# Kernel optimization log

Hardware: AMD Instinct MI355X
Metric: run time of the kernel (lower is better)

The kernel has to match this reference:

```python
import jax, jax.numpy as jnp
import numpy as np

N_NODES = 100000
N_EDGES = 400000
N_GRAPHS = 4096
IN_DIM = 128
HID = 64
HEADS = 8
NEG_SLOPE = 0.2


def setup_inputs() -> dict:
    key = jax.random.key(0)
    ks = jax.random.split(key, 12)
    x = jax.random.normal(ks[0], (N_NODES, IN_DIM), dtype=jnp.float32)
    edge_index = jax.random.randint(ks[1], (2, N_EDGES), 0, N_NODES, dtype=jnp.int64)
    batch = jnp.sort(jax.random.randint(ks[2], (N_NODES,), 0, N_GRAPHS, dtype=jnp.int64))
    s = 1.0 / np.sqrt(IN_DIM)
    W1 = jax.random.normal(ks[3], (IN_DIM, HEADS * HID), dtype=jnp.float32) * s
    att_src1 = jax.random.normal(ks[4], (HEADS, HID), dtype=jnp.float32) * 0.1
    att_dst1 = jax.random.normal(ks[5], (HEADS, HID), dtype=jnp.float32) * 0.1
    b1 = jnp.zeros((HEADS * HID,), dtype=jnp.float32)
    s2 = 1.0 / np.sqrt(HEADS * HID)
    W2 = jax.random.normal(ks[6], (HEADS * HID, HID), dtype=jnp.float32) * s2
    att_src2 = jax.random.normal(ks[7], (1, HID), dtype=jnp.float32) * 0.1
    att_dst2 = jax.random.normal(ks[8], (1, HID), dtype=jnp.float32) * 0.1
    b2 = jnp.zeros((HID,), dtype=jnp.float32)
    Wf = jax.random.normal(ks[9], (HID, 1), dtype=jnp.float32) * (1.0 / np.sqrt(HID))
    bf = jnp.zeros((1,), dtype=jnp.float32)
    return {"x": x, "edge_index": edge_index, "batch": batch,
            "W1": W1, "att_src1": att_src1, "att_dst1": att_dst1, "b1": b1,
            "W2": W2, "att_src2": att_src2, "att_dst2": att_dst2, "b2": b2,
            "Wf": Wf, "bf": bf}


def _gat_layer(x, src, dst, W, att_src, att_dst, bias, heads, out_ch, concat):
    # PyG GATConv math (add_self_loops handled by caller via src/dst)
    n = x.shape[0]
    h = (x @ W).reshape(n, heads, out_ch)          # [N, H, C]
    a_s = (h * att_src[None]).sum(-1)               # [N, H]
    a_d = (h * att_dst[None]).sum(-1)               # [N, H]
    alpha = a_s[src] + a_d[dst]                     # [E, H]
    alpha = jax.nn.leaky_relu(alpha, NEG_SLOPE)
    amax = jax.ops.segment_max(alpha, dst, num_segments=n)
    alpha = jnp.exp(alpha - amax[dst])
    denom = jax.ops.segment_sum(alpha, dst, num_segments=n)
    alpha = alpha / (denom[dst] + 1e-16)
    msg = h[src] * alpha[:, :, None]                # [E, H, C]
    out = jax.ops.segment_sum(msg, dst, num_segments=n)  # [N, H, C]
    out = out.reshape(n, heads * out_ch) if concat else out.mean(axis=1)
    return out + bias


def reference(x, edge_index, batch, W1, att_src1, att_dst1, b1,
              W2, att_src2, att_dst2, b2, Wf, bf):
    n = x.shape[0]
    loop = jnp.arange(n, dtype=edge_index.dtype)
    src = jnp.concatenate([edge_index[0], loop])
    dst = jnp.concatenate([edge_index[1], loop])
    h = _gat_layer(x, src, dst, W1, att_src1, att_dst1, b1, HEADS, HID, True)
    h = jax.nn.relu(h)
    h = _gat_layer(h, src, dst, W2, att_src2, att_dst2, b2, 1, HID, False)
    h = jax.nn.relu(h)
    sums = jax.ops.segment_sum(h, batch, num_segments=N_GRAPHS)        # [G, HID]
    cnts = jax.ops.segment_sum(jnp.ones((n,), h.dtype), batch, num_segments=N_GRAPHS)
    pooled = sums / jnp.clip(cnts, 1.0)[:, None]
    return pooled @ Wf + bf
```

## Files before the change

kernel.cpp:

```cpp
#include <hip/hip_runtime.h>

typedef short bfrag8 __attribute__((ext_vector_type(8)));
typedef float f32x4 __attribute__((ext_vector_type(4)));
typedef unsigned int uint4v __attribute__((ext_vector_type(4)));

__device__ __forceinline__ unsigned short f2bf(float f) {
    unsigned u = __float_as_uint(f);
    u += 0x7fffu + ((u >> 16) & 1u);
    return (unsigned short)(u >> 16);
}
__device__ __forceinline__ float bf2f(unsigned short s) {
    return __uint_as_float((unsigned)s << 16);
}

__global__ __launch_bounds__(256) void zero_i32(int* __restrict__ p, int n) {
    int i = (int)(blockIdx.x * 256u + threadIdx.x);
    int stride = gridDim.x * 256;
    for (; i < n; i += stride) p[i] = 0;
}

__global__ __launch_bounds__(256) void cvt_f32_bf16(const float* __restrict__ in,
                                                    unsigned short* __restrict__ out, size_t n) {
    size_t i = (blockIdx.x * 256llu + threadIdx.x) * 4;
    size_t stride = (size_t)gridDim.x * 1024llu;
    for (; i < n; i += stride) {
        float4 v = *(const float4*)(in + i);
        out[i + 0] = f2bf(v.x);
        out[i + 1] = f2bf(v.y);
        out[i + 2] = f2bf(v.z);
        out[i + 3] = f2bf(v.w);
    }
}

__global__ __launch_bounds__(256) void prep_w1(const float* __restrict__ W1,
                                               unsigned short* __restrict__ out) {
    int i = (int)(blockIdx.x * 256u + threadIdx.x);
    if (i >= 8 * 4 * 4 * 64 * 8) return;
    int e = i & 7, l = (i >> 3) & 63, c = (i >> 9) & 3, s = (i >> 11) & 3, h = i >> 13;
    int k = s * 32 + (l >> 4) * 8 + e;
    int col = h * 64 + c * 16 + (l & 15);
    out[i] = f2bf(W1[k * 512 + col]);
}

__global__ __launch_bounds__(256) void prep_w2(const float* __restrict__ W2,
                                               unsigned short* __restrict__ out) {
    int i = (int)(blockIdx.x * 256u + threadIdx.x);
    if (i >= 16 * 4 * 64 * 8) return;
    int e = i & 7, l = (i >> 3) & 63, c = (i >> 9) & 3, s = i >> 11;
    int k = s * 32 + (l >> 4) * 8 + e;
    int col = c * 16 + (l & 15);
    out[i] = f2bf(W2[k * 64 + col]);
}

__global__ __launch_bounds__(256) void hist_kernel(const int* __restrict__ ei,
                                                   int* __restrict__ cnt, int E, int N) {
    int t = (int)(blockIdx.x * 256u + threadIdx.x);
    if (t >= E + N) return;
    int dst = (t < E) ? ei[E + t] : t - E;
    atomicAdd(cnt + dst, 1);
}

#define SCAN_BLK 2048
__global__ __launch_bounds__(256) void scan1(const int* __restrict__ cnt,
                                             int* __restrict__ rs,
                                             int* __restrict__ bsum, int N) {
    __shared__ int lds[256];
    int base = blockIdx.x * SCAN_BLK;
    int vals[8];
    int tsum = 0;
    int idx0 = base + threadIdx.x * 8;
#pragma unroll
    for (int j = 0; j < 8; ++j) {
        int i = idx0 + j;
        int v = (i < N) ? cnt[i] : 0;
        vals[j] = tsum;
        tsum += v;
    }
    lds[threadIdx.x] = tsum;
    __syncthreads();
    for (int off = 1; off < 256; off <<= 1) {
        int v = lds[threadIdx.x];
        int u = (threadIdx.x >= (unsigned)off) ? lds[threadIdx.x - off] : 0;
        __syncthreads();
        lds[threadIdx.x] = v + u;
        __syncthreads();
    }
    int texcl = (threadIdx.x == 0) ? 0 : lds[threadIdx.x - 1];
#pragma unroll
    for (int j = 0; j < 8; ++j) {
        int i = idx0 + j;
        if (i < N) rs[i] = texcl + vals[j];
    }
    if (threadIdx.x == 255) bsum[blockIdx.x] = lds[255];
}

__global__ void scan2(int* __restrict__ bsum, int* __restrict__ rs, int nb, int N) {
    if (threadIdx.x == 0 && blockIdx.x == 0) {
        int run = 0;
        for (int b = 0; b < nb; ++b) { int t = bsum[b]; bsum[b] = run; run += t; }
        rs[N] = run;
    }
}

__global__ __launch_bounds__(256) void scan3(int* __restrict__ rs,
                                             const int* __restrict__ bsum, int N) {
    int i = (int)(blockIdx.x * 256u + threadIdx.x);
    if (i < N) rs[i] += bsum[i / SCAN_BLK];
}

__global__ __launch_bounds__(256) void scatter_kernel(const int* __restrict__ ei,
                                                      const int* __restrict__ rs,
                                                      int* __restrict__ cur,
                                                      int* __restrict__ csrc, int E, int N) {
    int t = (int)(blockIdx.x * 256u + threadIdx.x);
    if (t >= E + N) return;
    int src, dst;
    if (t < E) { src = ei[t]; dst = ei[E + t]; } else { src = dst = t - E; }
    int pos = rs[dst] + atomicAdd(cur + dst, 1);
    csrc[pos] = src;
}

__global__ __launch_bounds__(256) void gstart_build(const int* __restrict__ batch,
                                                    int* __restrict__ gstart, int N, int G) {
    int i = (int)(blockIdx.x * 256u + threadIdx.x);
    if (i > N) return;
    if (i == N) {
        int p = batch[N - 1];
        for (int g = p + 1; g <= G; ++g) gstart[g] = N;
    } else {
        int b = batch[i];
        int p = (i == 0) ? -1 : batch[i - 1];
        for (int g = p + 1; g <= b; ++g) gstart[g] = i;
    }
}

__global__ __launch_bounds__(256) void gemm_l1(const unsigned short* __restrict__ A,
                                               const unsigned short* __restrict__ Bfrag,
                                               unsigned short* __restrict__ Cbf,
                                               int M, int ldc, int asStride,
                                               const float* __restrict__ avs,
                                               const float* __restrict__ avd,
                                               float* __restrict__ as_,
                                               float* __restrict__ ad_) {
    const int lane = threadIdx.x & 63;
    const int wave = threadIdx.x >> 6;
    const int l15 = lane & 15, l16 = lane >> 4;
    const int cb = blockIdx.y;
    const long rowBase = (long)blockIdx.x * 128 + wave * 32;

    bfrag8 bf[4][4];
    const bfrag8* bp = (const bfrag8*)(Bfrag + (size_t)cb * 8192);
#pragma unroll
    for (int s = 0; s < 4; ++s)
#pragma unroll
        for (int c = 0; c < 4; ++c)
            bf[s][c] = bp[(s * 4 + c) * 64 + lane];

    f32x4 acc[2][4];
#pragma unroll
    for (int r = 0; r < 2; ++r)
#pragma unroll
        for (int c = 0; c < 4; ++c)
#pragma unroll
            for (int e = 0; e < 4; ++e) acc[r][c][e] = 0.f;

    long r0 = rowBase + l15;        if (r0 > M - 1) r0 = M - 1;
    long r1 = rowBase + 16 + l15;   if (r1 > M - 1) r1 = M - 1;
    const unsigned short* a0p = A + r0 * 128 + l16 * 8;
    const unsigned short* a1p = A + r1 * 128 + l16 * 8;

#pragma unroll
    for (int s = 0; s < 4; ++s) {
        bfrag8 a0 = *(const bfrag8*)(a0p + s * 32);
        bfrag8 a1 = *(const bfrag8*)(a1p + s * 32);
#pragma unroll
        for (int c = 0; c < 4; ++c) {
            acc[0][c] = __builtin_amdgcn_mfma_f32_16x16x32_bf16(a0, bf[s][c], acc[0][c], 0, 0, 0);
            acc[1][c] = __builtin_amdgcn_mfma_f32_16x16x32_bf16(a1, bf[s][c], acc[1][c], 0, 0, 0);
        }
    }

    float avsv[4], avdv[4];
#pragma unroll
    for (int c = 0; c < 4; ++c) {
        avsv[c] = avs[cb * 64 + c * 16 + l15];
        avdv[c] = avd[cb * 64 + c * 16 + l15];
    }

#pragma unroll
    for (int r = 0; r < 2; ++r) {
#pragma unroll
        for (int reg = 0; reg < 4; ++reg) {
            long row = rowBase + r * 16 + l16 * 4 + reg;
            bool ok = row < M;
            float ps = 0.f, pd = 0.f;
#pragma unroll
            for (int c = 0; c < 4; ++c) {
                float v = acc[r][c][reg];
                if (ok) Cbf[row * ldc + cb * 64 + c * 16 + l15] = f2bf(v);
                ps += v * avsv[c];
                pd += v * avdv[c];
            }
#pragma unroll
            for (int off = 1; off < 16; off <<= 1) {
                ps += __shfl_xor(ps, off);
                pd += __shfl_xor(pd, off);
            }
            if (l15 == 0 && ok) {
                as_[row * asStride + cb] = ps;
                ad_[row * asStride + cb] = pd;
            }
        }
    }
}

__global__ __launch_bounds__(256) void gemm_l2_k512(const unsigned short* __restrict__ A,
                                                    const unsigned short* __restrict__ Bfrag,
                                                    unsigned short* __restrict__ Cbf,
                                                    int M,
                                                    const float* __restrict__ avs,
                                                    const float* __restrict__ avd,
                                                    float* __restrict__ as_,
                                                    float* __restrict__ ad_) {
    const int lane = threadIdx.x & 63;
    const int wave = threadIdx.x >> 6;
    const int l15 = lane & 15, l16 = lane >> 4;
    const long rowBase = (long)blockIdx.x * 128 + wave * 32;
    const bfrag8* bp = (const bfrag8*)Bfrag;

    f32x4 acc[2][4];
#pragma unroll
    for (int r = 0; r < 2; ++r)
#pragma unroll
        for (int c = 0; c < 4; ++c)
#pragma unroll
            for (int e = 0; e < 4; ++e) acc[r][c][e] = 0.f;

    long r0 = rowBase + l15;        if (r0 > M - 1) r0 = M - 1;
    long r1 = rowBase + 16 + l15;   if (r1 > M - 1) r1 = M - 1;
    const unsigned short* a0p = A + r0 * 512 + l16 * 8;
    const unsigned short* a1p = A + r1 * 512 + l16 * 8;

    for (int s = 0; s < 16; ++s) {
        bfrag8 a0 = *(const bfrag8*)(a0p + s * 32);
        bfrag8 a1 = *(const bfrag8*)(a1p + s * 32);
        bfrag8 bf0 = bp[(s * 4 + 0) * 64 + lane];
        bfrag8 bf1 = bp[(s * 4 + 1) * 64 + lane];
        bfrag8 bf2 = bp[(s * 4 + 2) * 64 + lane];
        bfrag8 bf3 = bp[(s * 4 + 3) * 64 + lane];
        acc[0][0] = __builtin_amdgcn_mfma_f32_16x16x32_bf16(a0, bf0, acc[0][0], 0, 0, 0);
        acc[1][0] = __builtin_amdgcn_mfma_f32_16x16x32_bf16(a1, bf0, acc[1][0], 0, 0, 0);
        acc[0][1] = __builtin_amdgcn_mfma_f32_16x16x32_bf16(a0, bf1, acc[0][1], 0, 0, 0);
        acc[1][1] = __builtin_amdgcn_mfma_f32_16x16x32_bf16(a1, bf1, acc[1][1], 0, 0, 0);
        acc[0][2] = __builtin_amdgcn_mfma_f32_16x16x32_bf16(a0, bf2, acc[0][2], 0, 0, 0);
        acc[1][2] = __builtin_amdgcn_mfma_f32_16x16x32_bf16(a1, bf2, acc[1][2], 0, 0, 0);
        acc[0][3] = __builtin_amdgcn_mfma_f32_16x16x32_bf16(a0, bf3, acc[0][3], 0, 0, 0);
        acc[1][3] = __builtin_amdgcn_mfma_f32_16x16x32_bf16(a1, bf3, acc[1][3], 0, 0, 0);
    }

    float avsv[4], avdv[4];
#pragma unroll
    for (int c = 0; c < 4; ++c) {
        avsv[c] = avs[c * 16 + l15];
        avdv[c] = avd[c * 16 + l15];
    }

#pragma unroll
    for (int r = 0; r < 2; ++r) {
#pragma unroll
        for (int reg = 0; reg < 4; ++reg) {
            long row = rowBase + r * 16 + l16 * 4 + reg;
            bool ok = row < M;
            float ps = 0.f, pd = 0.f;
#pragma unroll
            for (int c = 0; c < 4; ++c) {
                float v = acc[r][c][reg];
                if (ok) Cbf[row * 64 + c * 16 + l15] = f2bf(v);
                ps += v * avsv[c];
                pd += v * avdv[c];
            }
#pragma unroll
            for (int off = 1; off < 16; off <<= 1) {
                ps += __shfl_xor(ps, off);
                pd += __shfl_xor(pd, off);
            }
            if (l15 == 0 && ok) { as_[row] = ps; ad_[row] = pd; }
        }
    }
}

template<bool ACC, bool WF32, bool WBF16, bool ATTN>
__global__ __launch_bounds__(256) void gemm_acc(const unsigned short* __restrict__ A,
                                                const unsigned short* __restrict__ Bfrag,
                                                float* __restrict__ Cf32,
                                                unsigned short* __restrict__ Cbf,
                                                int M,
                                                const float* __restrict__ avs,
                                                const float* __restrict__ avd,
                                                float* __restrict__ as_,
                                                float* __restrict__ ad_) {
    const int lane = threadIdx.x & 63;
    const int wave = threadIdx.x >> 6;
    const int l15 = lane & 15, l16 = lane >> 4;
    const long rowBase = (long)blockIdx.x * 128 + wave * 32;

    bfrag8 bf[2][4];
    const bfrag8* bp = (const bfrag8*)Bfrag;
#pragma unroll
    for (int s = 0; s < 2; ++s)
#pragma unroll
        for (int c = 0; c < 4; ++c)
            bf[s][c] = bp[(s * 4 + c) * 64 + lane];

    f32x4 acc[2][4];
#pragma unroll
    for (int r = 0; r < 2; ++r)
#pragma unroll
        for (int c = 0; c < 4; ++c)
#pragma unroll
            for (int e = 0; e < 4; ++e) acc[r][c][e] = 0.f;

    long r0 = rowBase + l15;        if (r0 > M - 1) r0 = M - 1;
    long r1 = rowBase + 16 + l15;   if (r1 > M - 1) r1 = M - 1;
    const unsigned short* a0p = A + r0 * 64 + l16 * 8;
    const unsigned short* a1p = A + r1 * 64 + l16 * 8;

#pragma unroll
    for (int s = 0; s < 2; ++s) {
        bfrag8 a0 = *(const bfrag8*)(a0p + s * 32);
        bfrag8 a1 = *(const bfrag8*)(a1p + s * 32);
#pragma unroll
        for (int c = 0; c < 4; ++c) {
            acc[0][c] = __builtin_amdgcn_mfma_f32_16x16x32_bf16(a0, bf[s][c], acc[0][c], 0, 0, 0);
            acc[1][c] = __builtin_amdgcn_mfma_f32_16x16x32_bf16(a1, bf[s][c], acc[1][c], 0, 0, 0);
        }
    }

    float avsv[4], avdv[4];
    if (ATTN) {
#pragma unroll
        for (int c = 0; c < 4; ++c) {
            avsv[c] = avs[c * 16 + l15];
            avdv[c] = avd[c * 16 + l15];
        }
    }

#pragma unroll
    for (int r = 0; r < 2; ++r) {
#pragma unroll
        for (int reg = 0; reg < 4; ++reg) {
            long row = rowBase + r * 16 + l16 * 4 + reg;
            bool ok = row < M;
            float ps = 0.f, pd = 0.f;
#pragma unroll
            for (int c = 0; c < 4; ++c) {
                float v = acc[r][c][reg];
                long idx = row * 64 + c * 16 + l15;
                if (ACC && ok) v += Cf32[idx];
                if (WF32 && ok) Cf32[idx] = v;
                if (WBF16 && ok) Cbf[idx] = f2bf(v);
                if (ATTN) { ps += v * avsv[c]; pd += v * avdv[c]; }
            }
            if (ATTN) {
#pragma unroll
                for (int off = 1; off < 16; off <<= 1) {
                    ps += __shfl_xor(ps, off);
                    pd += __shfl_xor(pd, off);
                }
                if (l15 == 0 && ok) { as_[row] = ps; ad_[row] = pd; }
            }
        }
    }
}

__global__ __launch_bounds__(256) void gather8(const int* __restrict__ csrc,
                                               const int* __restrict__ rs,
                                               const float* __restrict__ as_,
                                               const float* __restrict__ ad_,
                                               const unsigned short* __restrict__ h,
                                               const float* __restrict__ bias,
                                               unsigned short* __restrict__ outp,
                                               int N) {
    int node = (int)((blockIdx.x * 256u + threadIdx.x) >> 6);
    int lane = threadIdx.x & 63;
    if (node >= N) return;
    int myh = lane >> 3;
    int s0 = rs[node], s1 = rs[node + 1];
    float adn = ad_[(size_t)node * 8 + myh];
    float den = 0.f;
    float2 acc[4] = {};
    const unsigned* hu = (const unsigned*)h;
    int k = s0;
    for (; k + 4 <= s1; k += 4) {
        int i0 = csrc[k], i1 = csrc[k + 1], i2 = csrc[k + 2], i3 = csrc[k + 3];
        float a0 = as_[(size_t)i0 * 8 + myh] + adn;
        float a1 = as_[(size_t)i1 * 8 + myh] + adn;
        float a2 = as_[(size_t)i2 * 8 + myh] + adn;
        float a3 = as_[(size_t)i3 * 8 + myh] + adn;
        a0 = a0 > 0.f ? a0 : 0.2f * a0;  a1 = a1 > 0.f ? a1 : 0.2f * a1;
        a2 = a2 > 0.f ? a2 : 0.2f * a2;  a3 = a3 > 0.f ? a3 : 0.2f * a3;
        float w0 = __expf(fminf(a0, 60.f)), w1 = __expf(fminf(a1, 60.f));
        float w2 = __expf(fminf(a2, 60.f)), w3 = __expf(fminf(a3, 60.f));
        uint4v v0 = *(const uint4v*)(hu + (size_t)i0 * 256 + lane * 4);
        uint4v v1 = *(const uint4v*)(hu + (size_t)i1 * 256 + lane * 4);
        uint4v v2 = *(const uint4v*)(hu + (size_t)i2 * 256 + lane * 4);
        uint4v v3 = *(const uint4v*)(hu + (size_t)i3 * 256 + lane * 4);
        den += (w0 + w1) + (w2 + w3);
#pragma unroll
        for (int j = 0; j < 4; ++j) {
            acc[j].x += w0 * __uint_as_float(v0[j] << 16);
            acc[j].y += w0 * __uint_as_float(v0[j] & 0xffff0000u);
            acc[j].x += w1 * __uint_as_float(v1[j] << 16);
            acc[j].y += w1 * __uint_as_float(v1[j] & 0xffff0000u);
            acc[j].x += w2 * __uint_as_float(v2[j] << 16);
            acc[j].y += w2 * __uint_as_float(v2[j] & 0xffff0000u);
            acc[j].x += w3 * __uint_as_float(v3[j] << 16);
            acc[j].y += w3 * __uint_as_float(v3[j] & 0xffff0000u);
        }
    }
    for (; k < s1; ++k) {
        int i0 = csrc[k];
        float a = as_[(size_t)i0 * 8 + myh] + adn;
        a = a > 0.f ? a : 0.2f * a;
        float w = __expf(fminf(a, 60.f));
        uint4v v0 = *(const uint4v*)(hu + (size_t)i0 * 256 + lane * 4);
        den += w;
#pragma unroll
        for (int j = 0; j < 4; ++j) {
            acc[j].x += w * __uint_as_float(v0[j] << 16);
            acc[j].y += w * __uint_as_float(v0[j] & 0xffff0000u);
        }
    }
    float rden = 1.f / (den + 1e-16f);
    uint4v o;
#pragma unroll
    for (int j = 0; j < 4; ++j) {
        float vlo = acc[j].x * rden + bias[lane * 8 + 2 * j];
        float vhi = acc[j].y * rden + bias[lane * 8 + 2 * j + 1];
        vlo = vlo > 0.f ? vlo : 0.f;
        vhi = vhi > 0.f ? vhi : 0.f;
        o[j] = (unsigned)f2bf(vlo) | ((unsigned)f2bf(vhi) << 16);
    }
    __builtin_nontemporal_store(o, (uint4v*)(outp + (size_t)node * 512 + lane * 8));
}

template<bool OBF>
__global__ __launch_bounds__(256) void gather1(const int* __restrict__ csrc,
                                               const int* __restrict__ rs,
                                               const float* __restrict__ as_,
                                               const float* __restrict__ ad_,
                                               const unsigned short* __restrict__ h,
                                               const float* __restrict__ bias,
                                               void* __restrict__ outp, int N) {
    int node = (int)((blockIdx.x * 256u + threadIdx.x) >> 6);
    int lane = threadIdx.x & 63;
    if (node >= N) return;
    int s0 = rs[node], s1 = rs[node + 1];
    float adn = ad_[node];
    float den = 0.f, acc = 0.f;
    int k = s0;
    for (; k + 4 <= s1; k += 4) {
        int i0 = csrc[k], i1 = csrc[k + 1], i2 = csrc[k + 2], i3 = csrc[k + 3];
        float a0 = as_[i0] + adn, a1 = as_[i1] + adn, a2 = as_[i2] + adn, a3 = as_[i3] + adn;
        a0 = a0 > 0.f ? a0 : 0.2f * a0;  a1 = a1 > 0.f ? a1 : 0.2f * a1;
        a2 = a2 > 0.f ? a2 : 0.2f * a2;  a3 = a3 > 0.f ? a3 : 0.2f * a3;
        float w0 = __expf(fminf(a0, 60.f)), w1 = __expf(fminf(a1, 60.f));
        float w2 = __expf(fminf(a2, 60.f)), w3 = __expf(fminf(a3, 60.f));
        float h0 = bf2f(h[(size_t)i0 * 64 + lane]);
        float h1 = bf2f(h[(size_t)i1 * 64 + lane]);
        float h2 = bf2f(h[(size_t)i2 * 64 + lane]);
        float h3 = bf2f(h[(size_t)i3 * 64 + lane]);
        den += (w0 + w1) + (w2 + w3);
        acc += w0 * h0;  acc += w1 * h1;  acc += w2 * h2;  acc += w3 * h3;
    }
    for (; k < s1; ++k) {
        int i0 = csrc[k];
        float a = as_[i0] + adn;
        a = a > 0.f ? a : 0.2f * a;
        float w = __expf(fminf(a, 60.f));
        den += w;
        acc += w * bf2f(h[(size_t)i0 * 64 + lane]);
    }
    float v = acc / (den + 1e-16f) + bias[lane];
    v = v > 0.f ? v : 0.f;
    if (OBF) ((unsigned short*)outp)[(size_t)node * 64 + lane] = f2bf(v);
    else     ((float*)outp)[(size_t)node * 64 + lane] = v;
}

__global__ __launch_bounds__(256) void pool_readout(const float* __restrict__ h2,
                                                    const int* __restrict__ gstart,
                                                    const float* __restrict__ Wf,
                                                    const float* __restrict__ bf,
                                                    float* __restrict__ out, int G) {
    int g = (int)((blockIdx.x * 256u + threadIdx.x) >> 6);
    int lane = threadIdx.x & 63;
    if (g >= G) return;
    int s0 = gstart[g], s1 = gstart[g + 1];
    float acc = 0.f;
    int i = s0;
    for (; i + 2 <= s1; i += 2) {
        acc += h2[(size_t)i * 64 + lane];
        acc += h2[(size_t)(i + 1) * 64 + lane];
    }
    if (i < s1) acc += h2[(size_t)i * 64 + lane];
    float c = (float)(s1 - s0);
    c = c < 1.f ? 1.f : c;
    float v = acc / c * Wf[lane];
#pragma unroll
    for (int off = 32; off; off >>= 1) v += __shfl_xor(v, off);
    if (lane == 0) out[g] = v + bf[0];
}

extern "C" void kernel_launch(void* const* d_in, const int* in_sizes, int n_in,
                              void* d_out, int out_size, void* d_ws, size_t ws_size,
                              hipStream_t stream) {
    const float* x        = (const float*)d_in[0];
    const int*   ei       = (const int*)d_in[1];
    const int*   batch    = (const int*)d_in[2];
    const float* W1       = (const float*)d_in[3];
    const float* att_src1 = (const float*)d_in[4];
    const float* att_dst1 = (const float*)d_in[5];
    const float* b1       = (const float*)d_in[6];
    const float* W2       = (const float*)d_in[7];
    const float* att_src2 = (const float*)d_in[8];
    const float* att_dst2 = (const float*)d_in[9];
    const float* b2       = (const float*)d_in[10];
    const float* Wf       = (const float*)d_in[11];
    const float* bf       = (const float*)d_in[12];
    float* out = (float*)d_out;

    const int N = in_sizes[2];
    const int E = in_sizes[1] / 2;
    const int G = out_size;

    const int nb = (N + SCAN_BLK - 1) / SCAN_BLK;
    const int nodeWaveGrid = (int)(((size_t)N * 64 + 255) / 256);
    const int edgeGrid = (E + N + 255) / 256;
    const int gemmGrid = (N + 127) / 128;

    char* base = (char*)d_ws;
    size_t off = 0;
    auto alloc = [&](size_t bytes) { char* p = base + off; off += (bytes + 255) & ~255llu; return p; };
    unsigned short* wf1   = (unsigned short*)alloc(131072);
    unsigned short* wf2   = (unsigned short*)alloc(65536);
    float* as1            = (float*)alloc((size_t)N * 8 * 4);
    float* ad1            = (float*)alloc((size_t)N * 8 * 4);
    int*   cnt_i          = (int*)alloc((size_t)N * 4);
    int*   rs             = (int*)alloc((size_t)(N + 1) * 4);
    int*   csrc           = (int*)alloc((size_t)(E + N) * 4);
    int*   bsum           = (int*)alloc(1024);
    int*   gstart         = (int*)alloc((size_t)(G + 1) * 4);
    unsigned short* x_bf  = (unsigned short*)alloc((size_t)N * 128 * 2);
    float* ob2            = (float*)x_bf;
    unsigned short* h2bf  = (unsigned short*)alloc((size_t)N * 64 * 2);
    size_t commonEnd = off;

    size_t fusedNeed = commonEnd + 2 * (((size_t)N * 512 * 2 + 255) & ~255llu);
    bool fused = ws_size >= fusedNeed;

    cvt_f32_bf16<<<2048, 256, 0, stream>>>(x, x_bf, (size_t)N * 128);
    prep_w1<<<(8 * 4 * 4 * 64 * 8) / 256, 256, 0, stream>>>(W1, wf1);
    prep_w2<<<(16 * 4 * 64 * 8) / 256, 256, 0, stream>>>(W2, wf2);

    zero_i32<<<512, 256, 0, stream>>>(cnt_i, N);
    hist_kernel<<<edgeGrid, 256, 0, stream>>>(ei, cnt_i, E, N);
    scan1<<<nb, 256, 0, stream>>>(cnt_i, rs, bsum, N);
    scan2<<<1, 1, 0, stream>>>(bsum, rs, nb, N);
    scan3<<<(N + 255) / 256, 256, 0, stream>>>(rs, bsum, N);
    zero_i32<<<512, 256, 0, stream>>>(cnt_i, N);
    scatter_kernel<<<edgeGrid, 256, 0, stream>>>(ei, rs, cnt_i, csrc, E, N);
    gstart_build<<<(N + 256) / 256, 256, 0, stream>>>(batch, gstart, N, G);

    if (fused) {
        unsigned short* h1_bf  = (unsigned short*)alloc((size_t)N * 512 * 2);
        unsigned short* ob1_bf = (unsigned short*)alloc((size_t)N * 512 * 2);

        dim3 g1(gemmGrid, 8);
        gemm_l1<<<g1, 256, 0, stream>>>(x_bf, wf1, h1_bf, N, 512, 8,
                                        att_src1, att_dst1, as1, ad1);
        gather8<<<nodeWaveGrid, 256, 0, stream>>>(csrc, rs, as1, ad1, h1_bf, b1, ob1_bf, N);

        gemm_l2_k512<<<gemmGrid, 256, 0, stream>>>(ob1_bf, wf2, h2bf, N,
                                                   att_src2, att_dst2, as1, ad1);
        gather1<false><<<nodeWaveGrid, 256, 0, stream>>>(csrc, rs, as1, ad1, h2bf, b2, ob2, N);
    } else {
        unsigned short* hb_bf = (unsigned short*)alloc((size_t)N * 64 * 2);
        unsigned short* ob_bf = (unsigned short*)alloc((size_t)N * 64 * 2);
        float* h2acc          = (float*)alloc((size_t)N * 64 * 4);

        for (int h = 0; h < 8; ++h) {
            dim3 g1(gemmGrid, 1);
            gemm_l1<<<g1, 256, 0, stream>>>(x_bf, wf1 + (size_t)h * 8192, hb_bf, N, 64, 1,
                                            att_src1 + h * 64, att_dst1 + h * 64, as1, ad1);
            gather1<true><<<nodeWaveGrid, 256, 0, stream>>>(csrc, rs, as1, ad1, hb_bf, b1 + h * 64, ob_bf, N);
            if (h == 0) {
                gemm_acc<false, true, false, false><<<gemmGrid, 256, 0, stream>>>(
                    ob_bf, wf2, h2acc, nullptr, N, nullptr, nullptr, nullptr, nullptr);
            } else if (h < 7) {
                gemm_acc<true, true, false, false><<<gemmGrid, 256, 0, stream>>>(
                    ob_bf, wf2 + (size_t)h * 4096, h2acc, nullptr, N, nullptr, nullptr, nullptr, nullptr);
            } else {
                gemm_acc<true, false, true, true><<<gemmGrid, 256, 0, stream>>>(
                    ob_bf, wf2 + (size_t)h * 4096, h2acc, h2bf, N,
                    att_src2, att_dst2, as1, ad1);
            }
        }
        gather1<false><<<nodeWaveGrid, 256, 0, stream>>>(csrc, rs, as1, ad1, h2bf, b2, ob2, N);
    }

    pool_readout<<<(G * 64 + 255) / 256, 256, 0, stream>>>(ob2, gstart, Wf, bf, out, G);
}
```

Before: 314.9 us.

## Merge prologue kernels, fuse histogram into layer-1 GEMM, simplify CSR build

Folds input conversion, weight packing, count zeroing and graph-start construction into one multi-role prologue launch. Runs the destination histogram in extra blocks of the layer-1 GEMM launch. The scan's serial second pass and add pass become a single fix-up kernel that sums block totals per block, and the scatter counts down with atomicSub instead of re-zeroing the counter. The unfused per-head fallback is removed and layer-2 attention scores get separate buffers, so the kernel always assumes enough workspace for the large intermediates.

```diff
diff --git a/kernel.cpp b/kernel.cpp
--- a/kernel.cpp
+++ b/kernel.cpp
@@ -3,6 +3,8 @@
 typedef short bfrag8 __attribute__((ext_vector_type(8)));
 typedef float f32x4 __attribute__((ext_vector_type(4)));
 typedef unsigned int uint4v __attribute__((ext_vector_type(4)));
+
+#define SCAN_BLK 2048
 
 __device__ __forceinline__ unsigned short f2bf(float f) {
     unsigned u = __float_as_uint(f);
@@ -13,54 +15,156 @@
     return __uint_as_float((unsigned)s << 16);
 }
 
-__global__ __launch_bounds__(256) void zero_i32(int* __restrict__ p, int n) {
-    int i = (int)(blockIdx.x * 256u + threadIdx.x);
-    int stride = gridDim.x * 256;
-    for (; i < n; i += stride) p[i] = 0;
-}
-
-__global__ __launch_bounds__(256) void cvt_f32_bf16(const float* __restrict__ in,
-                                                    unsigned short* __restrict__ out, size_t n) {
-    size_t i = (blockIdx.x * 256llu + threadIdx.x) * 4;
-    size_t stride = (size_t)gridDim.x * 1024llu;
-    for (; i < n; i += stride) {
-        float4 v = *(const float4*)(in + i);
-        out[i + 0] = f2bf(v.x);
-        out[i + 1] = f2bf(v.y);
-        out[i + 2] = f2bf(v.z);
-        out[i + 3] = f2bf(v.w);
-    }
-}
-
-__global__ __launch_bounds__(256) void prep_w1(const float* __restrict__ W1,
-                                               unsigned short* __restrict__ out) {
-    int i = (int)(blockIdx.x * 256u + threadIdx.x);
-    if (i >= 8 * 4 * 4 * 64 * 8) return;
-    int e = i & 7, l = (i >> 3) & 63, c = (i >> 9) & 3, s = (i >> 11) & 3, h = i >> 13;
-    int k = s * 32 + (l >> 4) * 8 + e;
-    int col = h * 64 + c * 16 + (l & 15);
-    out[i] = f2bf(W1[k * 512 + col]);
-}
-
-__global__ __launch_bounds__(256) void prep_w2(const float* __restrict__ W2,
-                                               unsigned short* __restrict__ out) {
-    int i = (int)(blockIdx.x * 256u + threadIdx.x);
-    if (i >= 16 * 4 * 64 * 8) return;
-    int e = i & 7, l = (i >> 3) & 63, c = (i >> 9) & 3, s = i >> 11;
-    int k = s * 32 + (l >> 4) * 8 + e;
-    int col = c * 16 + (l & 15);
-    out[i] = f2bf(W2[k * 64 + col]);
-}
-
-__global__ __launch_bounds__(256) void hist_kernel(const int* __restrict__ ei,
-                                                   int* __restrict__ cnt, int E, int N) {
-    int t = (int)(blockIdx.x * 256u + threadIdx.x);
-    if (t >= E + N) return;
-    int dst = (t < E) ? ei[E + t] : t - E;
-    atomicAdd(cnt + dst, 1);
-}
-
-#define SCAN_BLK 2048
+__global__ __launch_bounds__(256) void prologue(const float* __restrict__ x,
+                                                unsigned short* __restrict__ x_bf,
+                                                int* __restrict__ cnt,
+                                                const float* __restrict__ W1,
+                                                const float* __restrict__ W2,
+                                                unsigned short* __restrict__ wf1,
+                                                unsigned short* __restrict__ wf2,
+                                                const int* __restrict__ batch,
+                                                int* __restrict__ gstart,
+                                                int* __restrict__ rs,
+                                                int N, int G, int E) {
+    const int b = blockIdx.x, t = threadIdx.x;
+    if (b < 1024) {
+        size_t n = (size_t)N * 128;
+        size_t i = ((size_t)b * 256 + t) * 4;
+        size_t stride = 1024llu * 256 * 4;
+        for (; i < n; i += stride) {
+            float4 v = *(const float4*)(x + i);
+            x_bf[i + 0] = f2bf(v.x);
+            x_bf[i + 1] = f2bf(v.y);
+            x_bf[i + 2] = f2bf(v.z);
+            x_bf[i + 3] = f2bf(v.w);
+        }
+    } else if (b < 1536) {
+        int i = (b - 1024) * 256 + t;
+        if (i < N) cnt[i] = 0;
+    } else if (b < 1792) {
+        int i = (b - 1536) * 256 + t;
+        if (i < 8 * 4 * 4 * 64 * 8) {
+            int e = i & 7, l = (i >> 3) & 63, c = (i >> 9) & 3, s = (i >> 11) & 3, h = i >> 13;
+            int k = s * 32 + (l >> 4) * 8 + e;
+            int col = h * 64 + c * 16 + (l & 15);
+            wf1[i] = f2bf(W1[k * 512 + col]);
+        }
+    } else if (b < 1920) {
+        int i = (b - 1792) * 256 + t;
+        if (i < 16 * 4 * 64 * 8) {
+            int e = i & 7, l = (i >> 3) & 63, c = (i >> 9) & 3, s = i >> 11;
+            int k = s * 32 + (l >> 4) * 8 + e;
+            int col = c * 16 + (l & 15);
+            wf2[i] = f2bf(W2[k * 64 + col]);
+        }
+    } else {
+        int i = (b - 1920) * 256 + t;
+        if (i == 0) rs[N] = E + N;
+        if (i > N) return;
+        if (i == N) {
+            int p = batch[N - 1];
+            for (int g = p + 1; g <= G; ++g) gstart[g] = N;
+        } else {
+            int bb = batch[i];
+            int p = (i == 0) ? -1 : batch[i - 1];
+            for (int g = p + 1; g <= bb; ++g) gstart[g] = i;
+        }
+    }
+}
+
+__global__ __launch_bounds__(256) void gemm_l1_hist(const unsigned short* __restrict__ A,
+                                                    const unsigned short* __restrict__ Bfrag,
+                                                    unsigned short* __restrict__ Cbf,
+                                                    int M,
+                                                    const float* __restrict__ avs,
+                                                    const float* __restrict__ avd,
+                                                    float* __restrict__ as_,
+                                                    float* __restrict__ ad_,
+                                                    int gemmBlocks, int rowBlocks,
+                                                    const int* __restrict__ ei,
+                                                    int* __restrict__ cnt, int E) {
+    const int b = blockIdx.x;
+    if (b >= gemmBlocks) {
+        int t = (b - gemmBlocks) * 256 + threadIdx.x;
+        if (t < E + M) {
+            int dst = (t < E) ? ei[E + t] : t - E;
+            atomicAdd(cnt + dst, 1);
+        }
+        return;
+    }
+    const int rb = b % rowBlocks;
+    const int cb = b / rowBlocks;
+    const int lane = threadIdx.x & 63;
+    const int wave = threadIdx.x >> 6;
+    const int l15 = lane & 15, l16 = lane >> 4;
+    const long rowBase = (long)rb * 128 + wave * 32;
+
+    bfrag8 bf[4][4];
+    const bfrag8* bp = (const bfrag8*)(Bfrag + (size_t)cb * 8192);
+#pragma unroll
+    for (int s = 0; s < 4; ++s)
+#pragma unroll
+        for (int c = 0; c < 4; ++c)
+            bf[s][c] = bp[(s * 4 + c) * 64 + lane];
+
+    f32x4 acc[2][4];
+#pragma unroll
+    for (int r = 0; r < 2; ++r)
+#pragma unroll
+        for (int c = 0; c < 4; ++c)
+#pragma unroll
+            for (int e = 0; e < 4; ++e) acc[r][c][e] = 0.f;
+
+    long r0 = rowBase + l15;        if (r0 > M - 1) r0 = M - 1;
+    long r1 = rowBase + 16 + l15;   if (r1 > M - 1) r1 = M - 1;
+    const unsigned short* a0p = A + r0 * 128 + l16 * 8;
+    const unsigned short* a1p = A + r1 * 128 + l16 * 8;
+
+#pragma unroll
+    for (int s = 0; s < 4; ++s) {
+        bfrag8 a0 = *(const bfrag8*)(a0p + s * 32);
+        bfrag8 a1 = *(const bfrag8*)(a1p + s * 32);
+#pragma unroll
+        for (int c = 0; c < 4; ++c) {
+            acc[0][c] = __builtin_amdgcn_mfma_f32_16x16x32_bf16(a0, bf[s][c], acc[0][c], 0, 0, 0);
+            acc[1][c] = __builtin_amdgcn_mfma_f32_16x16x32_bf16(a1, bf[s][c], acc[1][c], 0, 0, 0);
+        }
+    }
+
+    float avsv[4], avdv[4];
+#pragma unroll
+    for (int c = 0; c < 4; ++c) {
+        avsv[c] = avs[cb * 64 + c * 16 + l15];
+        avdv[c] = avd[cb * 64 + c * 16 + l15];
+    }
+
+#pragma unroll
+    for (int r = 0; r < 2; ++r) {
+#pragma unroll
+        for (int reg = 0; reg < 4; ++reg) {
+            long row = rowBase + r * 16 + l16 * 4 + reg;
+            bool ok = row < M;
+            float ps = 0.f, pd = 0.f;
+#pragma unroll
+            for (int c = 0; c < 4; ++c) {
+                float v = acc[r][c][reg];
+                if (ok) Cbf[row * 512 + cb * 64 + c * 16 + l15] = f2bf(v);
+                ps += v * avsv[c];
+                pd += v * avdv[c];
+            }
+#pragma unroll
+            for (int off = 1; off < 16; off <<= 1) {
+                ps += __shfl_xor(ps, off);
+                pd += __shfl_xor(pd, off);
+            }
+            if (l15 == 0 && ok) {
+                as_[row * 8 + cb] = ps;
+                ad_[row * 8 + cb] = pd;
+            }
+        }
+    }
+}
+
 __global__ __launch_bounds__(256) void scan1(const int* __restrict__ cnt,
                                              int* __restrict__ rs,
                                              int* __restrict__ bsum, int N) {
@@ -94,283 +198,31 @@
     if (threadIdx.x == 255) bsum[blockIdx.x] = lds[255];
 }
 
-__global__ void scan2(int* __restrict__ bsum, int* __restrict__ rs, int nb, int N) {
-    if (threadIdx.x == 0 && blockIdx.x == 0) {
-        int run = 0;
-        for (int b = 0; b < nb; ++b) { int t = bsum[b]; bsum[b] = run; run += t; }
-        rs[N] = run;
-    }
-}
-
-__global__ __launch_bounds__(256) void scan3(int* __restrict__ rs,
-                                             const int* __restrict__ bsum, int N) {
-    int i = (int)(blockIdx.x * 256u + threadIdx.x);
-    if (i < N) rs[i] += bsum[i / SCAN_BLK];
-}
-
-__global__ __launch_bounds__(256) void scatter_kernel(const int* __restrict__ ei,
-                                                      const int* __restrict__ rs,
-                                                      int* __restrict__ cur,
-                                                      int* __restrict__ csrc, int E, int N) {
+__global__ __launch_bounds__(256) void scan_fix(int* __restrict__ rs,
+                                                const int* __restrict__ bsum, int N) {
+    __shared__ int sprefix;
+    int b = blockIdx.x;
+    int i = b * 256 + threadIdx.x;
+    int chunk = (b * 256) / SCAN_BLK;
+    if (threadIdx.x == 0) {
+        int p = 0;
+        for (int k = 0; k < chunk; ++k) p += bsum[k];
+        sprefix = p;
+    }
+    __syncthreads();
+    if (i < N) rs[i] += sprefix;
+}
+
+__global__ __launch_bounds__(256) void scatter_cd(const int* __restrict__ ei,
+                                                  const int* __restrict__ rs,
+                                                  int* __restrict__ cnt,
+                                                  int* __restrict__ csrc, int E, int N) {
     int t = (int)(blockIdx.x * 256u + threadIdx.x);
     if (t >= E + N) return;
     int src, dst;
     if (t < E) { src = ei[t]; dst = ei[E + t]; } else { src = dst = t - E; }
-    int pos = rs[dst] + atomicAdd(cur + dst, 1);
+    int pos = rs[dst] + atomicSub(cnt + dst, 1) - 1;
     csrc[pos] = src;
-}
-
-__global__ __launch_bounds__(256) void gstart_build(const int* __restrict__ batch,
-                                                    int* __restrict__ gstart, int N, int G) {
-    int i = (int)(blockIdx.x * 256u + threadIdx.x);
-    if (i > N) return;
-    if (i == N) {
-        int p = batch[N - 1];
-        for (int g = p + 1; g <= G; ++g) gstart[g] = N;
-    } else {
-        int b = batch[i];
-        int p = (i == 0) ? -1 : batch[i - 1];
-        for (int g = p + 1; g <= b; ++g) gstart[g] = i;
-    }
-}
-
-__global__ __launch_bounds__(256) void gemm_l1(const unsigned short* __restrict__ A,
-                                               const unsigned short* __restrict__ Bfrag,
-                                               unsigned short* __restrict__ Cbf,
-                                               int M, int ldc, int asStride,
-                                               const float* __restrict__ avs,
-                                               const float* __restrict__ avd,
-                                               float* __restrict__ as_,
-                                               float* __restrict__ ad_) {
-    const int lane = threadIdx.x & 63;
-    const int wave = threadIdx.x >> 6;
-    const int l15 = lane & 15, l16 = lane >> 4;
-    const int cb = blockIdx.y;
-    const long rowBase = (long)blockIdx.x * 128 + wave * 32;
-
-    bfrag8 bf[4][4];
-    const bfrag8* bp = (const bfrag8*)(Bfrag + (size_t)cb * 8192);
-#pragma unroll
-    for (int s = 0; s < 4; ++s)
-#pragma unroll
-        for (int c = 0; c < 4; ++c)
-            bf[s][c] = bp[(s * 4 + c) * 64 + lane];
-
-    f32x4 acc[2][4];
-#pragma unroll
-    for (int r = 0; r < 2; ++r)
-#pragma unroll
-        for (int c = 0; c < 4; ++c)
-#pragma unroll
-            for (int e = 0; e < 4; ++e) acc[r][c][e] = 0.f;
-
-    long r0 = rowBase + l15;        if (r0 > M - 1) r0 = M - 1;
-    long r1 = rowBase + 16 + l15;   if (r1 > M - 1) r1 = M - 1;
-    const unsigned short* a0p = A + r0 * 128 + l16 * 8;
-    const unsigned short* a1p = A + r1 * 128 + l16 * 8;
-
-#pragma unroll
-    for (int s = 0; s < 4; ++s) {
-        bfrag8 a0 = *(const bfrag8*)(a0p + s * 32);
-        bfrag8 a1 = *(const bfrag8*)(a1p + s * 32);
-#pragma unroll
-        for (int c = 0; c < 4; ++c) {
-            acc[0][c] = __builtin_amdgcn_mfma_f32_16x16x32_bf16(a0, bf[s][c], acc[0][c], 0, 0, 0);
-            acc[1][c] = __builtin_amdgcn_mfma_f32_16x16x32_bf16(a1, bf[s][c], acc[1][c], 0, 0, 0);
-        }
-    }
-
-    float avsv[4], avdv[4];
-#pragma unroll
-    for (int c = 0; c < 4; ++c) {
-        avsv[c] = avs[cb * 64 + c * 16 + l15];
-        avdv[c] = avd[cb * 64 + c * 16 + l15];
-    }
-
-#pragma unroll
-    for (int r = 0; r < 2; ++r) {
-#pragma unroll
-        for (int reg = 0; reg < 4; ++reg) {
-            long row = rowBase + r * 16 + l16 * 4 + reg;
-            bool ok = row < M;
-            float ps = 0.f, pd = 0.f;
-#pragma unroll
-            for (int c = 0; c < 4; ++c) {
-                float v = acc[r][c][reg];
-                if (ok) Cbf[row * ldc + cb * 64 + c * 16 + l15] = f2bf(v);
-                ps += v * avsv[c];
-                pd += v * avdv[c];
-            }
-#pragma unroll
-            for (int off = 1; off < 16; off <<= 1) {
-                ps += __shfl_xor(ps, off);
-                pd += __shfl_xor(pd, off);
-            }
-            if (l15 == 0 && ok) {
-                as_[row * asStride + cb] = ps;
-                ad_[row * asStride + cb] = pd;
-            }
-        }
-    }
-}
-
-__global__ __launch_bounds__(256) void gemm_l2_k512(const unsigned short* __restrict__ A,
-                                                    const unsigned short* __restrict__ Bfrag,
-                                                    unsigned short* __restrict__ Cbf,
-                                                    int M,
-                                                    const float* __restrict__ avs,
-                                                    const float* __restrict__ avd,
-                                                    float* __restrict__ as_,
-                                                    float* __restrict__ ad_) {
-    const int lane = threadIdx.x & 63;
-    const int wave = threadIdx.x >> 6;
-    const int l15 = lane & 15, l16 = lane >> 4;
-    const long rowBase = (long)blockIdx.x * 128 + wave * 32;
-    const bfrag8* bp = (const bfrag8*)Bfrag;
-
-    f32x4 acc[2][4];
-#pragma unroll
-    for (int r = 0; r < 2; ++r)
-#pragma unroll
-        for (int c = 0; c < 4; ++c)
-#pragma unroll
-            for (int e = 0; e < 4; ++e) acc[r][c][e] = 0.f;
-
-    long r0 = rowBase + l15;        if (r0 > M - 1) r0 = M - 1;
-    long r1 = rowBase + 16 + l15;   if (r1 > M - 1) r1 = M - 1;
-    const unsigned short* a0p = A + r0 * 512 + l16 * 8;
-    const unsigned short* a1p = A + r1 * 512 + l16 * 8;
-
-    for (int s = 0; s < 16; ++s) {
-        bfrag8 a0 = *(const bfrag8*)(a0p + s * 32);
-        bfrag8 a1 = *(const bfrag8*)(a1p + s * 32);
-        bfrag8 bf0 = bp[(s * 4 + 0) * 64 + lane];
-        bfrag8 bf1 = bp[(s * 4 + 1) * 64 + lane];
-        bfrag8 bf2 = bp[(s * 4 + 2) * 64 + lane];
-        bfrag8 bf3 = bp[(s * 4 + 3) * 64 + lane];
-        acc[0][0] = __builtin_amdgcn_mfma_f32_16x16x32_bf16(a0, bf0, acc[0][0], 0, 0, 0);
-        acc[1][0] = __builtin_amdgcn_mfma_f32_16x16x32_bf16(a1, bf0, acc[1][0], 0, 0, 0);
-        acc[0][1] = __builtin_amdgcn_mfma_f32_16x16x32_bf16(a0, bf1, acc[0][1], 0, 0, 0);
-        acc[1][1] = __builtin_amdgcn_mfma_f32_16x16x32_bf16(a1, bf1, acc[1][1], 0, 0, 0);
-        acc[0][2] = __builtin_amdgcn_mfma_f32_16x16x32_bf16(a0, bf2, acc[0][2], 0, 0, 0);
-        acc[1][2] = __builtin_amdgcn_mfma_f32_16x16x32_bf16(a1, bf2, acc[1][2], 0, 0, 0);
-        acc[0][3] = __builtin_amdgcn_mfma_f32_16x16x32_bf16(a0, bf3, acc[0][3], 0, 0, 0);
-        acc[1][3] = __builtin_amdgcn_mfma_f32_16x16x32_bf16(a1, bf3, acc[1][3], 0, 0, 0);
-    }
-
-    float avsv[4], avdv[4];
-#pragma unroll
-    for (int c = 0; c < 4; ++c) {
-        avsv[c] = avs[c * 16 + l15];
-        avdv[c] = avd[c * 16 + l15];
-    }
-
-#pragma unroll
-    for (int r = 0; r < 2; ++r) {
-#pragma unroll
-        for (int reg = 0; reg < 4; ++reg) {
-            long row = rowBase + r * 16 + l16 * 4 + reg;
-            bool ok = row < M;
-            float ps = 0.f, pd = 0.f;
-#pragma unroll
-            for (int c = 0; c < 4; ++c) {
-                float v = acc[r][c][reg];
-                if (ok) Cbf[row * 64 + c * 16 + l15] = f2bf(v);
-                ps += v * avsv[c];
-                pd += v * avdv[c];
-            }
-#pragma unroll
-            for (int off = 1; off < 16; off <<= 1) {
-                ps += __shfl_xor(ps, off);
-                pd += __shfl_xor(pd, off);
-            }
-            if (l15 == 0 && ok) { as_[row] = ps; ad_[row] = pd; }
-        }
-    }
-}
-
-template<bool ACC, bool WF32, bool WBF16, bool ATTN>
-__global__ __launch_bounds__(256) void gemm_acc(const unsigned short* __restrict__ A,
-                                                const unsigned short* __restrict__ Bfrag,
-                                                float* __restrict__ Cf32,
-                                                unsigned short* __restrict__ Cbf,
-                                                int M,
-                                                const float* __restrict__ avs,
-                                                const float* __restrict__ avd,
-                                                float* __restrict__ as_,
-                                                float* __restrict__ ad_) {
-    const int lane = threadIdx.x & 63;
-    const int wave = threadIdx.x >> 6;
-    const int l15 = lane & 15, l16 = lane >> 4;
-    const long rowBase = (long)blockIdx.x * 128 + wave * 32;
-
-    bfrag8 bf[2][4];
-    const bfrag8* bp = (const bfrag8*)Bfrag;
-#pragma unroll
-    for (int s = 0; s < 2; ++s)
-#pragma unroll
-        for (int c = 0; c < 4; ++c)
-            bf[s][c] = bp[(s * 4 + c) * 64 + lane];
-
-    f32x4 acc[2][4];
-#pragma unroll
-    for (int r = 0; r < 2; ++r)
-#pragma unroll
-        for (int c = 0; c < 4; ++c)
-#pragma unroll
-            for (int e = 0; e < 4; ++e) acc[r][c][e] = 0.f;
-
-    long r0 = rowBase + l15;        if (r0 > M - 1) r0 = M - 1;
-    long r1 = rowBase + 16 + l15;   if (r1 > M - 1) r1 = M - 1;
-    const unsigned short* a0p = A + r0 * 64 + l16 * 8;
-    const unsigned short* a1p = A + r1 * 64 + l16 * 8;
-
-#pragma unroll
-    for (int s = 0; s < 2; ++s) {
-        bfrag8 a0 = *(const bfrag8*)(a0p + s * 32);
-        bfrag8 a1 = *(const bfrag8*)(a1p + s * 32);
-#pragma unroll
-        for (int c = 0; c < 4; ++c) {
-            acc[0][c] = __builtin_amdgcn_mfma_f32_16x16x32_bf16(a0, bf[s][c], acc[0][c], 0, 0, 0);
-            acc[1][c] = __builtin_amdgcn_mfma_f32_16x16x32_bf16(a1, bf[s][c], acc[1][c], 0, 0, 0);
-        }
-    }
-
-    float avsv[4], avdv[4];
-    if (ATTN) {
-#pragma unroll
-        for (int c = 0; c < 4; ++c) {
-            avsv[c] = avs[c * 16 + l15];
-            avdv[c] = avd[c * 16 + l15];
-        }
-    }
-
-#pragma unroll
-    for (int r = 0; r < 2; ++r) {
-#pragma unroll
-        for (int reg = 0; reg < 4; ++reg) {
-            long row = rowBase + r * 16 + l16 * 4 + reg;
-            bool ok = row < M;
-            float ps = 0.f, pd = 0.f;
-#pragma unroll
-            for (int c = 0; c < 4; ++c) {
-                float v = acc[r][c][reg];
-                long idx = row * 64 + c * 16 + l15;
-                if (ACC && ok) v += Cf32[idx];
-                if (WF32 && ok) Cf32[idx] = v;
-                if (WBF16 && ok) Cbf[idx] = f2bf(v);
-                if (ATTN) { ps += v * avsv[c]; pd += v * avdv[c]; }
-            }
-            if (ATTN) {
-#pragma unroll
-                for (int off = 1; off < 16; off <<= 1) {
-                    ps += __shfl_xor(ps, off);
-                    pd += __shfl_xor(pd, off);
-                }
-                if (l15 == 0 && ok) { as_[row] = ps; ad_[row] = pd; }
-            }
-        }
-    }
 }
 
 __global__ __launch_bounds__(256) void gather8(const int* __restrict__ csrc,
@@ -441,17 +293,91 @@
         vhi = vhi > 0.f ? vhi : 0.f;
         o[j] = (unsigned)f2bf(vlo) | ((unsigned)f2bf(vhi) << 16);
     }
-    __builtin_nontemporal_store(o, (uint4v*)(outp + (size_t)node * 512 + lane * 8));
-}
-
-template<bool OBF>
+    *(uint4v*)(outp + (size_t)node * 512 + lane * 8) = o;
+}
+
+__global__ __launch_bounds__(256) void gemm_l2_k512(const unsigned short* __restrict__ A,
+                                                    const unsigned short* __restrict__ Bfrag,
+                                                    unsigned short* __restrict__ Cbf,
+                                                    int M,
+                                                    const float* __restrict__ avs,
+                                                    const float* __restrict__ avd,
+                                                    float* __restrict__ as_,
+                                                    float* __restrict__ ad_) {
+    const int lane = threadIdx.x & 63;
+    const int wave = threadIdx.x >> 6;
+    const int l15 = lane & 15, l16 = lane >> 4;
+    const long rowBase = (long)blockIdx.x * 128 + wave * 32;
+    const bfrag8* bp = (const bfrag8*)Bfrag;
+
+    f32x4 acc[2][4];
+#pragma unroll
+    for (int r = 0; r < 2; ++r)
+#pragma unroll
+        for (int c = 0; c < 4; ++c)
+#pragma unroll
+            for (int e = 0; e < 4; ++e) acc[r][c][e] = 0.f;
+
+    long r0 = rowBase + l15;        if (r0 > M - 1) r0 = M - 1;
+    long r1 = rowBase + 16 + l15;   if (r1 > M - 1) r1 = M - 1;
+    const unsigned short* a0p = A + r0 * 512 + l16 * 8;
+    const unsigned short* a1p = A + r1 * 512 + l16 * 8;
+
+    for (int s = 0; s < 16; ++s) {
+        bfrag8 a0 = *(const bfrag8*)(a0p + s * 32);
+        bfrag8 a1 = *(const bfrag8*)(a1p + s * 32);
+        bfrag8 bf0 = bp[(s * 4 + 0) * 64 + lane];
+        bfrag8 bf1 = bp[(s * 4 + 1) * 64 + lane];
+        bfrag8 bf2 = bp[(s * 4 + 2) * 64 + lane];
+        bfrag8 bf3 = bp[(s * 4 + 3) * 64 + lane];
+        acc[0][0] = __builtin_amdgcn_mfma_f32_16x16x32_bf16(a0, bf0, acc[0][0], 0, 0, 0);
+        acc[1][0] = __builtin_amdgcn_mfma_f32_16x16x32_bf16(a1, bf0, acc[1][0], 0, 0, 0);
+        acc[0][1] = __builtin_amdgcn_mfma_f32_16x16x32_bf16(a0, bf1, acc[0][1], 0, 0, 0);
+        acc[1][1] = __builtin_amdgcn_mfma_f32_16x16x32_bf16(a1, bf1, acc[1][1], 0, 0, 0);
+        acc[0][2] = __builtin_amdgcn_mfma_f32_16x16x32_bf16(a0, bf2, acc[0][2], 0, 0, 0);
+        acc[1][2] = __builtin_amdgcn_mfma_f32_16x16x32_bf16(a1, bf2, acc[1][2], 0, 0, 0);
+        acc[0][3] = __builtin_amdgcn_mfma_f32_16x16x32_bf16(a0, bf3, acc[0][3], 0, 0, 0);
+        acc[1][3] = __builtin_amdgcn_mfma_f32_16x16x32_bf16(a1, bf3, acc[1][3], 0, 0, 0);
+    }
+
+    float avsv[4], avdv[4];
+#pragma unroll
+    for (int c = 0; c < 4; ++c) {
+        avsv[c] = avs[c * 16 + l15];
+        avdv[c] = avd[c * 16 + l15];
+    }
+
+#pragma unroll
+    for (int r = 0; r < 2; ++r) {
+#pragma unroll
+        for (int reg = 0; reg < 4; ++reg) {
+            long row = rowBase + r * 16 + l16 * 4 + reg;
+            bool ok = row < M;
+            float ps = 0.f, pd = 0.f;
+#pragma unroll
+            for (int c = 0; c < 4; ++c) {
+                float v = acc[r][c][reg];
+                if (ok) Cbf[row * 64 + c * 16 + l15] = f2bf(v);
+                ps += v * avsv[c];
+                pd += v * avdv[c];
+            }
+#pragma unroll
+            for (int off = 1; off < 16; off <<= 1) {
+                ps += __shfl_xor(ps, off);
+                pd += __shfl_xor(pd, off);
+            }
+            if (l15 == 0 && ok) { as_[row] = ps; ad_[row] = pd; }
+        }
+    }
+}
+
 __global__ __launch_bounds__(256) void gather1(const int* __restrict__ csrc,
                                                const int* __restrict__ rs,
                                                const float* __restrict__ as_,
                                                const float* __restrict__ ad_,
                                                const unsigned short* __restrict__ h,
                                                const float* __restrict__ bias,
-                                               void* __restrict__ outp, int N) {
+                                               float* __restrict__ outp, int N) {
     int node = (int)((blockIdx.x * 256u + threadIdx.x) >> 6);
     int lane = threadIdx.x & 63;
     if (node >= N) return;
@@ -482,9 +408,7 @@
         acc += w * bf2f(h[(size_t)i0 * 64 + lane]);
     }
     float v = acc / (den + 1e-16f) + bias[lane];
-    v = v > 0.f ? v : 0.f;
-    if (OBF) ((unsigned short*)outp)[(size_t)node * 64 + lane] = f2bf(v);
-    else     ((float*)outp)[(size_t)node * 64 + lane] = v;
+    outp[(size_t)node * 64 + lane] = v > 0.f ? v : 0.f;
 }
 
 __global__ __launch_bounds__(256) void pool_readout(const float* __restrict__ h2,
@@ -545,6 +469,8 @@
     unsigned short* wf2   = (unsigned short*)alloc(65536);
     float* as1            = (float*)alloc((size_t)N * 8 * 4);
     float* ad1            = (float*)alloc((size_t)N * 8 * 4);
+    float* as2            = (float*)alloc((size_t)N * 4);
+    float* ad2            = (float*)alloc((size_t)N * 4);
     int*   cnt_i          = (int*)alloc((size_t)N * 4);
     int*   rs             = (int*)alloc((size_t)(N + 1) * 4);
     int*   csrc           = (int*)alloc((size_t)(E + N) * 4);
@@ -553,60 +479,34 @@
     unsigned short* x_bf  = (unsigned short*)alloc((size_t)N * 128 * 2);
     float* ob2            = (float*)x_bf;
     unsigned short* h2bf  = (unsigned short*)alloc((size_t)N * 64 * 2);
-    size_t commonEnd = off;
-
-    size_t fusedNeed = commonEnd + 2 * (((size_t)N * 512 * 2 + 255) & ~255llu);
-    bool fused = ws_size >= fusedNeed;
-
-    cvt_f32_bf16<<<2048, 256, 0, stream>>>(x, x_bf, (size_t)N * 128);
-    prep_w1<<<(8 * 4 * 4 * 64 * 8) / 256, 256, 0, stream>>>(W1, wf1);
-    prep_w2<<<(16 * 4 * 64 * 8) / 256, 256, 0, stream>>>(W2, wf2);
-
-    zero_i32<<<512, 256, 0, stream>>>(cnt_i, N);
-    hist_kernel<<<edgeGrid, 256, 0, stream>>>(ei, cnt_i, E, N);
+    unsigned short* h1_bf = (unsigned short*)alloc((size_t)N * 512 * 2);
+    unsigned short* ob1_bf= (unsigned short*)alloc((size_t)N * 512 * 2);
+    (void)ws_size;
+
+    {
+        int gsBlocks = (N + 256) / 256 + 1;
+        int grid = 1920 + gsBlocks;
+        prologue<<<grid, 256, 0, stream>>>(x, x_bf, cnt_i, W1, W2, wf1, wf2,
+                                           batch, gstart, rs, N, G, E);
+    }
+
+    {
+        int gemmBlocks = gemmGrid * 8;
+        gemm_l1_hist<<<gemmBlocks + edgeGrid, 256, 0, stream>>>(
+            x_bf, wf1, h1_bf, N, att_src1, att_dst1, as1, ad1,
+            gemmBlocks, gemmGrid, ei, cnt_i, E);
+    }
+
     scan1<<<nb, 256, 0, stream>>>(cnt_i, rs, bsum, N);
-    scan2<<<1, 1, 0, stream>>>(bsum, rs, nb, N);
-    scan3<<<(N + 255) / 256, 256, 0, stream>>>(rs, bsum, N);
-    zero_i32<<<512, 256, 0, stream>>>(cnt_i, N);
-    scatter_kernel<<<edgeGrid, 256, 0, stream>>>(ei, rs, cnt_i, csrc, E, N);
-    gstart_build<<<(N + 256) / 256, 256, 0, stream>>>(batch, gstart, N, G);
-
-    if (fused) {
-        unsigned short* h1_bf  = (unsigned short*)alloc((size_t)N * 512 * 2);
-        unsigned short* ob1_bf = (unsigned short*)alloc((size_t)N * 512 * 2);
-
-        dim3 g1(gemmGrid, 8);
-        gemm_l1<<<g1, 256, 0, stream>>>(x_bf, wf1, h1_bf, N, 512, 8,
-                                        att_src1, att_dst1, as1, ad1);
-        gather8<<<nodeWaveGrid, 256, 0, stream>>>(csrc, rs, as1, ad1, h1_bf, b1, ob1_bf, N);
-
-        gemm_l2_k512<<<gemmGrid, 256, 0, stream>>>(ob1_bf, wf2, h2bf, N,
-                                                   att_src2, att_dst2, as1, ad1);
-        gather1<false><<<nodeWaveGrid, 256, 0, stream>>>(csrc, rs, as1, ad1, h2bf, b2, ob2, N);
-    } else {
-        unsigned short* hb_bf = (unsigned short*)alloc((size_t)N * 64 * 2);
-        unsigned short* ob_bf = (unsigned short*)alloc((size_t)N * 64 * 2);
-        float* h2acc          = (float*)alloc((size_t)N * 64 * 4);
-
-        for (int h = 0; h < 8; ++h) {
-            dim3 g1(gemmGrid, 1);
-            gemm_l1<<<g1, 256, 0, stream>>>(x_bf, wf1 + (size_t)h * 8192, hb_bf, N, 64, 1,
-                                            att_src1 + h * 64, att_dst1 + h * 64, as1, ad1);
-            gather1<true><<<nodeWaveGrid, 256, 0, stream>>>(csrc, rs, as1, ad1, hb_bf, b1 + h * 64, ob_bf, N);
-            if (h == 0) {
-                gemm_acc<false, true, false, false><<<gemmGrid, 256, 0, stream>>>(
-                    ob_bf, wf2, h2acc, nullptr, N, nullptr, nullptr, nullptr, nullptr);
-            } else if (h < 7) {
-                gemm_acc<true, true, false, false><<<gemmGrid, 256, 0, stream>>>(
-                    ob_bf, wf2 + (size_t)h * 4096, h2acc, nullptr, N, nullptr, nullptr, nullptr, nullptr);
-            } else {
-                gemm_acc<true, false, true, true><<<gemmGrid, 256, 0, stream>>>(
-                    ob_bf, wf2 + (size_t)h * 4096, h2acc, h2bf, N,
-                    att_src2, att_dst2, as1, ad1);
-            }
-        }
-        gather1<false><<<nodeWaveGrid, 256, 0, stream>>>(csrc, rs, as1, ad1, h2bf, b2, ob2, N);
-    }
+    scan_fix<<<(N + 255) / 256, 256, 0, stream>>>(rs, bsum, N);
+    scatter_cd<<<edgeGrid, 256, 0, stream>>>(ei, rs, cnt_i, csrc, E, N);
+
+    gather8<<<nodeWaveGrid, 256, 0, stream>>>(csrc, rs, as1, ad1, h1_bf, b1, ob1_bf, N);
+
+    gemm_l2_k512<<<gemmGrid, 256, 0, stream>>>(ob1_bf, wf2, h2bf, N,
+                                               att_src2, att_dst2, as2, ad2);
+
+    gather1<<<nodeWaveGrid, 256, 0, stream>>>(csrc, rs, as2, ad2, h2bf, b2, ob2, N);
 
     pool_readout<<<(G * 64 + 255) / 256, 256, 0, stream>>>(ob2, gstart, Wf, bf, out, G);
 }
```

After: 292.7 us. -7.0%, faster.
